# Performance work log

Measured on AMD Instinct MI355X. Metric: run time of the kernel, lower is better.

## Reference

```python
import jax, jax.numpy as jnp
import numpy as np
import math

G = 96        # grid cells per axis (domain_size)
N = 400000    # particles, one per occupied cell
CELL = 0.05   # cell size == particle radius parameter d


def setup_inputs():
    rng = np.random.default_rng(0)
    cells = rng.permutation(G ** 3)[:N]
    cz_i = cells // (G * G)
    cy_i = (cells // G) % G
    cx_i = cells % G
    key = jax.random.key(0)
    ks = jax.random.split(key, 6)

    def pos(k, idx):
        jitter = jax.random.uniform(k, (N,), minval=-0.3, maxval=0.3)
        return (jnp.asarray(idx, jnp.float32) + jitter) * CELL

    x = pos(ks[0], cx_i)
    y = pos(ks[1], cy_i)
    z = pos(ks[2], cz_i)
    vx = jax.random.normal(ks[3], (N,), jnp.float32) * 0.1
    vy = jax.random.normal(ks[4], (N,), jnp.float32) * 0.1
    vz = jax.random.normal(ks[5], (N,), jnp.float32) * 0.1
    restitution = 0.5
    alpha = -math.log(restitution) / math.pi
    gamma = alpha / math.sqrt(alpha ** 2 + 1.0)
    kn = 600000.0
    m = 4.0 / 3.0 * 3.1415 * CELL ** 3 * 2700.0
    eta = 2.0 * gamma * math.sqrt(kn * m / 2.0)
    return dict(
        compressed_x_grid=x, compressed_y_grid=y, compressed_z_grid=z,
        compressed_vx_grid=vx, compressed_vy_grid=vy, compressed_vz_grid=vz,
        d=CELL, kn=kn, damping_coefficient_Eta=eta,
        friction_coefficient=0.5, dt=0.001,
        input_shape=(1, 1, G, G, G), filter_size=5)


def reference(compressed_x_grid, compressed_y_grid, compressed_z_grid,
              compressed_vx_grid, compressed_vy_grid, compressed_vz_grid,
              d, kn, damping_coefficient_Eta, friction_coefficient, dt,
              input_shape, filter_size):
    Gz, Gy, Gx = input_shape[2], input_shape[3], input_shape[4]
    n = compressed_x_grid.shape[0]
    eps = jnp.float32(1e-4)
    two_d = 2.0 * d

    # cell indices (one particle per cell, as in the torch module)
    cx = jnp.round(compressed_x_grid / d).astype(jnp.int32)
    cy = jnp.round(compressed_y_grid / d).astype(jnp.int32)
    cz = jnp.round(compressed_z_grid / d).astype(jnp.int32)

    def scatter(v):
        return jnp.zeros((Gz, Gy, Gx), v.dtype).at[cz, cy, cx].set(v)

    xg = scatter(compressed_x_grid)
    yg = scatter(compressed_y_grid)
    zg = scatter(compressed_z_grid)
    vxg = scatter(compressed_vx_grid)
    vyg = scatter(compressed_vy_grid)
    vzg = scatter(compressed_vz_grid)

    half = filter_size // 2
    shifts = jnp.array([[kk - half, jj - half, ii - half]
                        for ii in range(filter_size)
                        for jj in range(filter_size)
                        for kk in range(filter_size)], dtype=jnp.int32)

    def body(carry, shift):
        fxc, fyc, fzc, fxd, fyd, fzd = carry

        def gat(g):
            r = jnp.roll(g, shift[0], axis=0)
            r = jnp.roll(r, shift[1], axis=1)
            r = jnp.roll(r, shift[2], axis=2)
            return r[cz, cy, cx]

        # diff = grid - rolled grid, gathered at the particle cells.
        # grid[cell] holds the particle's own value, so gather(self) == value.
        dx = compressed_x_grid - gat(xg)
        dy = compressed_y_grid - gat(yg)
        dz = compressed_z_grid - gat(zg)
        dvx = compressed_vx_grid - gat(vxg)
        dvy = compressed_vy_grid - gat(vyg)
        dvz = compressed_vz_grid - gat(vzg)

        dist = jnp.sqrt(dx * dx + dy * dy + dz * dz)
        den = jnp.maximum(eps, dist)
        vn = (dvx * dx + dvy * dy + dvz * dz) / den  # normal relative velocity
        ov = dist < two_d                            # overlap mask
        fcol = kn * (dist - two_d) / den             # Hookean repulsion / den
        fdmp = damping_coefficient_Eta * vn / den    # normal damping / den

        fxc = fxc + jnp.where(ov, fcol * dx, 0.0)
        fyc = fyc + jnp.where(ov, fcol * dy, 0.0)
        fzc = fzc + jnp.where(ov, fcol * dz, 0.0)
        fxd = fxd + jnp.where(ov, fdmp * dx, 0.0)
        fyd = fyd + jnp.where(ov, fdmp * dy, 0.0)
        fzd = fzd + jnp.where(ov, fdmp * dz, 0.0)
        return (fxc, fyc, fzc, fxd, fyd, fzd), None

    zeros = jnp.zeros((n,), jnp.float32)
    carry, _ = jax.lax.scan(body, (zeros, zeros, zeros, zeros, zeros, zeros), shifts)
    fxc, fyc, fzc, fxd, fyd, fzd = carry

    # wall (boundary) spring forces, domain extent = grid_dim * cell_size
    dsx, dsy, dsz = Gx * d, Gy * d, Gz * d

    def wall(p, ds):
        lo = jnp.where((p != 0.0) & (p < d), kn * (d - p), 0.0)
        hi = jnp.where(p > ds - two_d, kn * (p - ds + two_d), 0.0)
        return lo - hi

    fbx = wall(compressed_x_grid, dsx)
    fby = wall(compressed_y_grid, dsy)
    fbz = wall(compressed_z_grid, dsz)

    return jnp.stack([fxc, fyc, fzc, fxd, fyd, fzd, fbx, fby, fbz])
```

## Files before the change

### kernel.cpp

```cpp
#include <hip/hip_runtime.h>
#include <hip/hip_fp16.h>

#define GDIM 96
#define GCELLS (GDIM * GDIM * GDIM)
#define TILE 8
#define HALO 12
#define NT (GDIM / TILE)
#define HCELLS (HALO * HALO * HALO)
#define TCELLS (TILE * TILE * TILE)
#define EMPTY16 0xFBFBu
#define EMPTY32 0xFBFBFBFBu


constexpr int WT_[25] = {1,3,5,3,1, 3,5,5,5,3, 5,5,5,5,5, 3,5,5,5,3, 1,3,5,3,1};

__device__ inline float2 h2f(unsigned int u) {
    union { unsigned int u; __half2 h; } c; c.u = u;
    return __half22float2(c.h);
}
__device__ inline unsigned int f2h(float a, float b) {
    union { __half2 h; unsigned int u; } c; c.h = __floats2half2_rn(a, b);
    return c.u;
}

__global__ __launch_bounds__(256) void scatter_k(
    const float* __restrict__ x, const float* __restrict__ y, const float* __restrict__ z,
    const float* __restrict__ vx, const float* __restrict__ vy, const float* __restrict__ vz,
    const float* __restrict__ dp, const float* __restrict__ knp,
    uint4* __restrict__ grid, float* __restrict__ out, int n)
{
    int i = blockIdx.x * blockDim.x + threadIdx.x;
    if (i >= n) return;
    float d = dp[0], kn = knp[0];
    float invd = 1.0f / d;
    float fx = x[i], fy = y[i], fz = z[i];
    int cx = __float2int_rn(fx * invd);
    int cy = __float2int_rn(fy * invd);
    int cz = __float2int_rn(fz * invd);
    float jx = fmaf(fx, invd, -(float)cx);
    float jy = fmaf(fy, invd, -(float)cy);
    float jz = fmaf(fz, invd, -(float)cz);

    uint4 rec;
    rec.x = f2h(jx, jy);
    rec.y = f2h(jz, vx[i]);
    rec.z = f2h(vy[i], vz[i]);
    rec.w = (unsigned int)(i + 1);
    grid[(size_t)(cz * GDIM + cy) * GDIM + cx] = rec;

    float two_d = 2.0f * d, ds = (float)GDIM * d;
    size_t N = (size_t)n;
    float lox = (fx != 0.0f && fx < d) ? kn * (d - fx) : 0.0f;
    float hix = (fx > ds - two_d) ? kn * (fx - ds + two_d) : 0.0f;
    float loy = (fy != 0.0f && fy < d) ? kn * (d - fy) : 0.0f;
    float hiy = (fy > ds - two_d) ? kn * (fy - ds + two_d) : 0.0f;
    float loz = (fz != 0.0f && fz < d) ? kn * (d - fz) : 0.0f;
    float hiz = (fz > ds - two_d) ? kn * (fz - ds + two_d) : 0.0f;
    out[6 * N + i] = lox - hix;
    out[7 * N + i] = loy - hiy;
    out[8 * N + i] = loz - hiz;
}

__global__ __launch_bounds__(256, 6) void force_tile_k(
    const uint4* __restrict__ grid,
    const float* __restrict__ dp, const float* __restrict__ knp,
    const float* __restrict__ etap, float* __restrict__ out, int n)
{
    __shared__ uint2 JA[HCELLS];
    __shared__ unsigned int VV[HCELLS];
    __shared__ unsigned int llist[TCELLS];
    __shared__ int lcount;

    int tid = threadIdx.x;
    int tileid = blockIdx.x;
    int tx = tileid % NT;
    int ty = (tileid / NT) % NT;
    int tz = tileid / (NT * NT);
    int bx = tx * TILE - 2, by = ty * TILE - 2, bz = tz * TILE - 2;

    if (tid == 0) lcount = 0;
    __syncthreads();

    int lane = tid & 63;
    for (int h = tid; h < HCELLS; h += 256) {
        int hx = h % HALO;
        int hy = (h / HALO) % HALO;
        int hz = h / (HALO * HALO);
        int ux = bx + hx, uy = by + hy, uz = bz + hz;
        int gx = ux; if (gx < 0) gx += GDIM; else if (gx >= GDIM) gx -= GDIM;
        int gy = uy; if (gy < 0) gy += GDIM; else if (gy >= GDIM) gy -= GDIM;
        int gz = uz; if (gz < 0) gz += GDIM; else if (gz >= GDIM) gz -= GDIM;
        uint4 r = grid[(size_t)(gz * GDIM + gy) * GDIM + gx];
        bool occ_any = r.w != EMPTY32;
        int Wx = gx - ux, Wy = gy - uy, Wz = gz - uz;
        if (occ_any && ((Wx | Wy | Wz) != 0)) {
            float2 jxy = h2f(r.x), jzv = h2f(r.y);
            r.x = f2h(jxy.x + (float)Wx, jxy.y + (float)Wy);
            r.y = f2h(jzv.x + (float)Wz, jzv.y);
        }
        JA[h] = make_uint2(r.x, r.y);
        VV[h] = r.z;
        bool inter = hx >= 2 && hx < 2 + TILE && hy >= 2 && hy < 2 + TILE &&
                     hz >= 2 && hz < 2 + TILE;
        bool occ = inter && occ_any;
        unsigned long long m = __ballot(occ);
        int base = 0;
        if (lane == 0 && m) base = atomicAdd(&lcount, __popcll(m));
        base = __shfl(base, 0);
        if (occ) {
            int off = __popcll(m & ((1ull << lane) - 1ull));
            int ic = ((hz - 2) * TILE + (hy - 2)) * TILE + (hx - 2);
            llist[base + off] = (r.w << 9) | (unsigned int)ic;
        }
    }
    __syncthreads();

    float d = dp[0], kn = knp[0], eta = etap[0];
    int cnt = lcount;
    size_t N = (size_t)n;

    for (int i = tid; i < cnt; i += 256) {
        unsigned int e = llist[i];
        int lc = (int)(e & 511u);
        int pid = (int)(e >> 9) - 1;
        int lx = lc & 7, ly = (lc >> 3) & 7, lz = lc >> 6;
        int hc = ((lz + 2) * HALO + (ly + 2)) * HALO + (lx + 2);
        uint2 ja = JA[hc];
        float2 jxy = h2f(ja.x), jzw = h2f(ja.y), vyz = h2f(VV[hc]);
        float jxi = jxy.x, jyi = jxy.y, jzi = jzw.x;
        float vxi = jzw.y, vyi = vyz.x, vzi = vyz.y;

        float fxc = 0, fyc = 0, fzc = 0, fxd = 0, fyd = 0, fzd = 0;
#pragma unroll
        for (int iz = 0; iz < 5; ++iz) {
#pragma unroll
            for (int iy = 0; iy < 5; ++iy) {
                const int w = WT_[iz * 5 + iy];
                const int x0 = (5 - w) / 2;
                int rb = ((lz + iz) * HALO + (ly + iy)) * HALO + lx;
#pragma unroll
                for (int k = 0; k < w; ++k) {
                    const int ix = x0 + k;
                    int idx = rb + ix;
                    uint2 j2 = JA[idx];
                    float2 njxy = h2f(j2.x), njzw = h2f(j2.y), nvyz = h2f(VV[idx]);
                    float dx = (jxi - njxy.x) + (float)(2 - ix);
                    float dy = (jyi - njxy.y) + (float)(2 - iy);
                    float dz = (jzi - njzw.x) + (float)(2 - iz);
                    float dvx = vxi - njzw.y;
                    float dvy = vyi - nvyz.x;
                    float dvz = vzi - nvyz.y;
                    float s = fmaf(dx, dx, fmaf(dy, dy, dz * dz));
                    float t = fmaxf(s, 4e-6f);
                    float rinv = __builtin_amdgcn_rsqf(t);
                    float dist = s * rinv;
                    float dot = fmaf(dvx, dx, fmaf(dvy, dy, dvz * dz));
                    bool ov = dist < 2.0f;
                    float fc = ov ? (dist - 2.0f) * rinv : 0.0f;
                    float fd = ov ? dot * rinv * rinv : 0.0f;
                    fxc = fmaf(fc, dx, fxc); fyc = fmaf(fc, dy, fyc); fzc = fmaf(fc, dz, fzc);
                    fxd = fmaf(fd, dx, fxd); fyd = fmaf(fd, dy, fyd); fzd = fmaf(fd, dz, fzd);
                }
            }
        }

        float pxc = (float)(tx * TILE + lx) + jxi;
        float pyc = (float)(ty * TILE + ly) + jyi;
        float pzc = (float)(tz * TILE + lz) + jzi;
        float ss = pxc * pxc + pyc * pyc + pzc * pzc;
        if (ss < 4.0f) {
            int cntE = 0;
#pragma unroll 1
            for (int iz = 0; iz < 5; ++iz)
#pragma unroll 1
                for (int iy = 0; iy < 5; ++iy)
#pragma unroll 1
                    for (int ix = 0; ix < 5; ++ix) {
                        int hc2 = ((lz + iz) * HALO + (ly + iy)) * HALO + (lx + ix);
                        if ((JA[hc2].x & 0xFFFFu) == EMPTY16) ++cntE;
                    }
            if (cntE) {
                float t = fmaxf(ss, 4e-6f);
                float rinv = __builtin_amdgcn_rsqf(t);
                float dist = ss * rinv;
                if (dist < 2.0f) {
                    float fcE = (dist - 2.0f) * rinv;
                    float dotE = vxi * pxc + vyi * pyc + vzi * pzc;
                    float fdE = dotE * rinv * rinv;
                    float c = (float)cntE;
                    fxc = fmaf(c * fcE, pxc, fxc); fyc = fmaf(c * fcE, pyc, fyc); fzc = fmaf(c * fcE, pzc, fzc);
                    fxd = fmaf(c * fdE, pxc, fxd); fyd = fmaf(c * fdE, pyc, fyd); fzd = fmaf(c * fdE, pzc, fzd);
                }
            }
        }

        float kd = kn * d;
        out[0 * N + pid] = fxc * kd;
        out[1 * N + pid] = fyc * kd;
        out[2 * N + pid] = fzc * kd;
        out[3 * N + pid] = fxd * eta;
        out[4 * N + pid] = fyd * eta;
        out[5 * N + pid] = fzd * eta;
    }
}

extern "C" void kernel_launch(void* const* d_in, const int* in_sizes, int n_in,
                              void* d_out, int out_size, void* d_ws, size_t ws_size,
                              hipStream_t stream)
{
    const float* x  = (const float*)d_in[0];
    const float* y  = (const float*)d_in[1];
    const float* z  = (const float*)d_in[2];
    const float* vx = (const float*)d_in[3];
    const float* vy = (const float*)d_in[4];
    const float* vz = (const float*)d_in[5];
    const float* dp   = (const float*)d_in[6];
    const float* knp  = (const float*)d_in[7];
    const float* etap = (const float*)d_in[8];
    int n = in_sizes[0];

    uint4* grid = (uint4*)d_ws;

    hipMemsetAsync(d_ws, 0xFB, (size_t)GCELLS * 16, stream);

    int blocks = (n + 255) / 256;
    scatter_k<<<blocks, 256, 0, stream>>>(x, y, z, vx, vy, vz, dp, knp, grid, (float*)d_out, n);
    force_tile_k<<<NT * NT * NT, 256, 0, stream>>>(grid, dp, knp, etap, (float*)d_out, n);
}
```

Measured before the change: 82.31 us.

## Split stencil across two thread halves per particle with smaller 8x8x4 tiles

The force kernel now uses 8x8x4 tiles (12x12x8 halo) with 512 threads per block. Each occupied cell is handled by two threads, each covering about half of the 5x5x5 stencil rows, and the partial forces are combined through shared memory that reuses the halo buffer. Block IDs are also remapped in strides of 8. The goal is more parallelism and better latency hiding than one thread looping over the full stencil. The cost is a larger halo-to-interior ratio (more redundant global loads), an extra sync-and-reduce step, and imbalance because the wall-check branch runs only in the first half.

```diff
diff --git a/kernel.cpp b/kernel.cpp
--- a/kernel.cpp
+++ b/kernel.cpp
@@ -3,16 +3,18 @@
 
 #define GDIM 96
 #define GCELLS (GDIM * GDIM * GDIM)
-#define TILE 8
-#define HALO 12
-#define NT (GDIM / TILE)
-#define HCELLS (HALO * HALO * HALO)
-#define TCELLS (TILE * TILE * TILE)
+#define HX 12
+#define HY 12
+#define HZ 8
+#define HCELLS (HX * HY * HZ)
+#define TCELLS 256
+#define NTX 12
+#define NTY 12
+#define NTZ 24
+#define NBLK (NTX * NTY * NTZ)
 #define EMPTY16 0xFBFBu
 #define EMPTY32 0xFBFBFBFBu
 
-
-constexpr int WT_[25] = {1,3,5,3,1, 3,5,5,5,3, 5,5,5,5,5, 3,5,5,5,3, 1,3,5,3,1};
 
 __device__ inline float2 h2f(unsigned int u) {
     union { unsigned int u; __half2 h; } c; c.u = u;
@@ -61,31 +63,61 @@
     out[8 * N + i] = loz - hiz;
 }
 
-__global__ __launch_bounds__(256, 6) void force_tile_k(
+#define NROW(IZ, IY, W, X0) { \
+    int rb = ((lz + IZ) * HY + (ly + IY)) * HX + lx; \
+    _Pragma("unroll") \
+    for (int k = 0; k < W; ++k) { \
+        const int ix = X0 + k; \
+        int idx = rb + ix; \
+        uint2 j2 = JA[idx]; \
+        float2 njxy = h2f(j2.x), njzw = h2f(j2.y), nvyz = h2f(VV[idx]); \
+        float dx = (jxi - njxy.x) + (float)(2 - ix); \
+        float dy = (jyi - njxy.y) + (float)(2 - IY); \
+        float dz = (jzi - njzw.x) + (float)(2 - IZ); \
+        float dvx = vxi - njzw.y, dvy = vyi - nvyz.x, dvz = vzi - nvyz.y; \
+        float s = fmaf(dx, dx, fmaf(dy, dy, dz * dz)); \
+        float t = fmaxf(s, 4e-6f); \
+        float rinv = __builtin_amdgcn_rsqf(t); \
+        float dist = s * rinv; \
+        float dot = fmaf(dvx, dx, fmaf(dvy, dy, dvz * dz)); \
+        bool ov = dist < 2.0f; \
+        float fc = ov ? (dist - 2.0f) * rinv : 0.0f; \
+        float fd = ov ? dot * rinv * rinv : 0.0f; \
+        fxc = fmaf(fc, dx, fxc); fyc = fmaf(fc, dy, fyc); fzc = fmaf(fc, dz, fzc); \
+        fxd = fmaf(fd, dx, fxd); fyd = fmaf(fd, dy, fyd); fzd = fmaf(fd, dz, fzd); \
+    } }
+
+__global__ __launch_bounds__(512, 8) void force_tile_k(
     const uint4* __restrict__ grid,
     const float* __restrict__ dp, const float* __restrict__ knp,
     const float* __restrict__ etap, float* __restrict__ out, int n)
 {
-    __shared__ uint2 JA[HCELLS];
-    __shared__ unsigned int VV[HCELLS];
+    __shared__ union {
+        struct { uint2 JA[HCELLS]; unsigned int VV[HCELLS]; } g;
+        float pbuf[6 * TCELLS];
+    } U;
     __shared__ unsigned int llist[TCELLS];
     __shared__ int lcount;
 
+    uint2* JA = U.g.JA;
+    unsigned int* VV = U.g.VV;
+
     int tid = threadIdx.x;
-    int tileid = blockIdx.x;
-    int tx = tileid % NT;
-    int ty = (tileid / NT) % NT;
-    int tz = tileid / (NT * NT);
-    int bx = tx * TILE - 2, by = ty * TILE - 2, bz = tz * TILE - 2;
+    int bid = blockIdx.x;
+    int tileid = (bid & 7) * (NBLK / 8) + (bid >> 3);
+    int tx = tileid % NTX;
+    int ty = (tileid / NTX) % NTY;
+    int tz = tileid / (NTX * NTY);
+    int bx = tx * 8 - 2, by = ty * 8 - 2, bz = tz * 4 - 2;
 
     if (tid == 0) lcount = 0;
     __syncthreads();
 
     int lane = tid & 63;
-    for (int h = tid; h < HCELLS; h += 256) {
-        int hx = h % HALO;
-        int hy = (h / HALO) % HALO;
-        int hz = h / (HALO * HALO);
+    for (int h = tid; h < HCELLS; h += 512) {
+        int hx = h % HX;
+        int hy = (h / HX) % HY;
+        int hz = h / (HX * HY);
         int ux = bx + hx, uy = by + hy, uz = bz + hz;
         int gx = ux; if (gx < 0) gx += GDIM; else if (gx >= GDIM) gx -= GDIM;
         int gy = uy; if (gy < 0) gy += GDIM; else if (gy >= GDIM) gy -= GDIM;
@@ -100,8 +132,7 @@
         }
         JA[h] = make_uint2(r.x, r.y);
         VV[h] = r.z;
-        bool inter = hx >= 2 && hx < 2 + TILE && hy >= 2 && hy < 2 + TILE &&
-                     hz >= 2 && hz < 2 + TILE;
+        bool inter = hx >= 2 && hx < 10 && hy >= 2 && hy < 10 && hz >= 2 && hz < 6;
         bool occ = inter && occ_any;
         unsigned long long m = __ballot(occ);
         int base = 0;
@@ -109,8 +140,8 @@
         base = __shfl(base, 0);
         if (occ) {
             int off = __popcll(m & ((1ull << lane) - 1ull));
-            int ic = ((hz - 2) * TILE + (hy - 2)) * TILE + (hx - 2);
-            llist[base + off] = (r.w << 9) | (unsigned int)ic;
+            int ic = ((hz - 2) * 8 + (hy - 2)) * 8 + (hx - 2);
+            llist[base + off] = (r.w << 8) | (unsigned int)ic;
         }
     }
     __syncthreads();
@@ -118,89 +149,84 @@
     float d = dp[0], kn = knp[0], eta = etap[0];
     int cnt = lcount;
     size_t N = (size_t)n;
-
-    for (int i = tid; i < cnt; i += 256) {
-        unsigned int e = llist[i];
-        int lc = (int)(e & 511u);
-        int pid = (int)(e >> 9) - 1;
-        int lx = lc & 7, ly = (lc >> 3) & 7, lz = lc >> 6;
-        int hc = ((lz + 2) * HALO + (ly + 2)) * HALO + (lx + 2);
-        uint2 ja = JA[hc];
-        float2 jxy = h2f(ja.x), jzw = h2f(ja.y), vyz = h2f(VV[hc]);
-        float jxi = jxy.x, jyi = jxy.y, jzi = jzw.x;
-        float vxi = jzw.y, vyi = vyz.x, vzi = vyz.y;
-
-        float fxc = 0, fyc = 0, fzc = 0, fxd = 0, fyd = 0, fzd = 0;
-#pragma unroll
-        for (int iz = 0; iz < 5; ++iz) {
-#pragma unroll
-            for (int iy = 0; iy < 5; ++iy) {
-                const int w = WT_[iz * 5 + iy];
-                const int x0 = (5 - w) / 2;
-                int rb = ((lz + iz) * HALO + (ly + iy)) * HALO + lx;
-#pragma unroll
-                for (int k = 0; k < w; ++k) {
-                    const int ix = x0 + k;
-                    int idx = rb + ix;
-                    uint2 j2 = JA[idx];
-                    float2 njxy = h2f(j2.x), njzw = h2f(j2.y), nvyz = h2f(VV[idx]);
-                    float dx = (jxi - njxy.x) + (float)(2 - ix);
-                    float dy = (jyi - njxy.y) + (float)(2 - iy);
-                    float dz = (jzi - njzw.x) + (float)(2 - iz);
-                    float dvx = vxi - njzw.y;
-                    float dvy = vyi - nvyz.x;
-                    float dvz = vzi - nvyz.y;
-                    float s = fmaf(dx, dx, fmaf(dy, dy, dz * dz));
-                    float t = fmaxf(s, 4e-6f);
+    int base = tid & 255;
+    bool isg0 = tid < 256;
+    bool active = base < cnt;
+
+    int lc = 0, pid = -1;
+    if (active) {
+        unsigned int e = llist[base];
+        lc = (int)(e & 255u);
+        pid = (int)(e >> 8) - 1;
+    }
+    int lx = lc & 7, ly = (lc >> 3) & 7, lz = lc >> 6;
+    int hc = ((lz + 2) * HY + (ly + 2)) * HX + (lx + 2);
+    uint2 ja = JA[hc];
+    float2 jxy = h2f(ja.x), jzw = h2f(ja.y), vyz = h2f(VV[hc]);
+    float jxi = jxy.x, jyi = jxy.y, jzi = jzw.x;
+    float vxi = jzw.y, vyi = vyz.x, vzi = vyz.y;
+
+    float fxc = 0, fyc = 0, fzc = 0, fxd = 0, fyd = 0, fzd = 0;
+    if (active) {
+        if (isg0) {
+            NROW(0,0,1,2) NROW(0,1,3,1) NROW(0,2,5,0) NROW(0,3,3,1) NROW(0,4,1,2)
+            NROW(1,0,3,1) NROW(1,1,5,0) NROW(1,2,5,0) NROW(1,3,5,0) NROW(1,4,3,1)
+            NROW(2,0,5,0) NROW(2,1,5,0)
+
+            float pxc = (float)(tx * 8 + lx) + jxi;
+            float pyc = (float)(ty * 8 + ly) + jyi;
+            float pzc = (float)(tz * 4 + lz) + jzi;
+            float ss = pxc * pxc + pyc * pyc + pzc * pzc;
+            if (ss < 4.0f) {
+                int cntE = 0;
+#pragma unroll 1
+                for (int iz = 0; iz < 5; ++iz)
+#pragma unroll 1
+                    for (int iy = 0; iy < 5; ++iy)
+#pragma unroll 1
+                        for (int ix = 0; ix < 5; ++ix) {
+                            int hc2 = ((lz + iz) * HY + (ly + iy)) * HX + (lx + ix);
+                            if ((JA[hc2].x & 0xFFFFu) == EMPTY16) ++cntE;
+                        }
+                if (cntE) {
+                    float t = fmaxf(ss, 4e-6f);
                     float rinv = __builtin_amdgcn_rsqf(t);
-                    float dist = s * rinv;
-                    float dot = fmaf(dvx, dx, fmaf(dvy, dy, dvz * dz));
-                    bool ov = dist < 2.0f;
-                    float fc = ov ? (dist - 2.0f) * rinv : 0.0f;
-                    float fd = ov ? dot * rinv * rinv : 0.0f;
-                    fxc = fmaf(fc, dx, fxc); fyc = fmaf(fc, dy, fyc); fzc = fmaf(fc, dz, fzc);
-                    fxd = fmaf(fd, dx, fxd); fyd = fmaf(fd, dy, fyd); fzd = fmaf(fd, dz, fzd);
+                    float dist = ss * rinv;
+                    if (dist < 2.0f) {
+                        float fcE = (dist - 2.0f) * rinv;
+                        float dotE = vxi * pxc + vyi * pyc + vzi * pzc;
+                        float fdE = dotE * rinv * rinv;
+                        float c = (float)cntE;
+                        fxc = fmaf(c * fcE, pxc, fxc); fyc = fmaf(c * fcE, pyc, fyc); fzc = fmaf(c * fcE, pzc, fzc);
+                        fxd = fmaf(c * fdE, pxc, fxd); fyd = fmaf(c * fdE, pyc, fyd); fzd = fmaf(c * fdE, pzc, fzd);
+                    }
                 }
             }
+        } else {
+            NROW(2,2,5,0) NROW(2,3,5,0) NROW(2,4,5,0)
+            NROW(3,0,3,1) NROW(3,1,5,0) NROW(3,2,5,0) NROW(3,3,5,0) NROW(3,4,3,1)
+            NROW(4,0,1,2) NROW(4,1,3,1) NROW(4,2,5,0) NROW(4,3,3,1) NROW(4,4,1,2)
         }
-
-        float pxc = (float)(tx * TILE + lx) + jxi;
-        float pyc = (float)(ty * TILE + ly) + jyi;
-        float pzc = (float)(tz * TILE + lz) + jzi;
-        float ss = pxc * pxc + pyc * pyc + pzc * pzc;
-        if (ss < 4.0f) {
-            int cntE = 0;
-#pragma unroll 1
-            for (int iz = 0; iz < 5; ++iz)
-#pragma unroll 1
-                for (int iy = 0; iy < 5; ++iy)
-#pragma unroll 1
-                    for (int ix = 0; ix < 5; ++ix) {
-                        int hc2 = ((lz + iz) * HALO + (ly + iy)) * HALO + (lx + ix);
-                        if ((JA[hc2].x & 0xFFFFu) == EMPTY16) ++cntE;
-                    }
-            if (cntE) {
-                float t = fmaxf(ss, 4e-6f);
-                float rinv = __builtin_amdgcn_rsqf(t);
-                float dist = ss * rinv;
-                if (dist < 2.0f) {
-                    float fcE = (dist - 2.0f) * rinv;
-                    float dotE = vxi * pxc + vyi * pyc + vzi * pzc;
-                    float fdE = dotE * rinv * rinv;
-                    float c = (float)cntE;
-                    fxc = fmaf(c * fcE, pxc, fxc); fyc = fmaf(c * fcE, pyc, fyc); fzc = fmaf(c * fcE, pzc, fzc);
-                    fxd = fmaf(c * fdE, pxc, fxd); fyd = fmaf(c * fdE, pyc, fyd); fzd = fmaf(c * fdE, pzc, fzd);
-                }
-            }
-        }
-
+    }
+
+    __syncthreads();
+    if (!isg0 && active) {
+        U.pbuf[0 * TCELLS + base] = fxc;
+        U.pbuf[1 * TCELLS + base] = fyc;
+        U.pbuf[2 * TCELLS + base] = fzc;
+        U.pbuf[3 * TCELLS + base] = fxd;
+        U.pbuf[4 * TCELLS + base] = fyd;
+        U.pbuf[5 * TCELLS + base] = fzd;
+    }
+    __syncthreads();
+    if (isg0 && active) {
         float kd = kn * d;
-        out[0 * N + pid] = fxc * kd;
-        out[1 * N + pid] = fyc * kd;
-        out[2 * N + pid] = fzc * kd;
-        out[3 * N + pid] = fxd * eta;
-        out[4 * N + pid] = fyd * eta;
-        out[5 * N + pid] = fzd * eta;
+        out[0 * N + pid] = (fxc + U.pbuf[0 * TCELLS + base]) * kd;
+        out[1 * N + pid] = (fyc + U.pbuf[1 * TCELLS + base]) * kd;
+        out[2 * N + pid] = (fzc + U.pbuf[2 * TCELLS + base]) * kd;
+        out[3 * N + pid] = (fxd + U.pbuf[3 * TCELLS + base]) * eta;
+        out[4 * N + pid] = (fyd + U.pbuf[4 * TCELLS + base]) * eta;
+        out[5 * N + pid] = (fzd + U.pbuf[5 * TCELLS + base]) * eta;
     }
 }
 
@@ -225,5 +251,5 @@
 
     int blocks = (n + 255) / 256;
     scatter_k<<<blocks, 256, 0, stream>>>(x, y, z, vx, vy, vz, dp, knp, grid, (float*)d_out, n);
-    force_tile_k<<<NT * NT * NT, 256, 0, stream>>>(grid, dp, knp, etap, (float*)d_out, n);
-}
+    force_tile_k<<<NBLK, 512, 0, stream>>>(grid, dp, knp, etap, (float*)d_out, n);
+}
```

Result: slower. 90.84 us (+10.4%).
